# Performance work log

Measured on AMD Instinct MI355X. Metric: run time of the kernel, lower is better.

The kernel has to match this reference:

```python
import jax, jax.numpy as jnp
import numpy as np

IN_DIM = 4096
OUT_DIM = 4096
BLOCK = 256
RANK = 16
B_IN = IN_DIM // BLOCK   # 16
B_OUT = OUT_DIM // BLOCK # 16


def setup_inputs() -> dict:
    key = jax.random.key(0)
    k1, k2, k3, k4, k5 = jax.random.split(key, 5)
    x = jax.random.normal(k1, (2, 1024, IN_DIM), dtype=jnp.float32)
    # S ~ U[0, 2)
    S = jax.random.uniform(k2, (B_OUT, B_IN, RANK), dtype=jnp.float32, minval=0.0, maxval=2.0)
    std = np.sqrt(0.02).astype(np.float32)
    U = jax.random.normal(k3, (B_OUT, RANK, BLOCK), dtype=jnp.float32) * std
    Vt = jax.random.normal(k4, (B_IN, BLOCK, RANK), dtype=jnp.float32) * std
    # kaiming_uniform_ on a (1, out_dim) tensor with default a=sqrt(5): bound = 1/sqrt(fan_in) = 1/sqrt(out_dim)
    bound = float(1.0 / np.sqrt(OUT_DIM))
    bias = jax.random.uniform(k5, (OUT_DIM,), dtype=jnp.float32, minval=-bound, maxval=bound)
    return {"x": x, "S": S, "U": U, "Vt": Vt, "bias": bias}


def reference(x, S, U, Vt, bias):
    # Faithful to Blast.forward: it reconstructs the dense weight by running
    # forward2 on an identity matrix (which ALSO adds bias to every row of W),
    # then computes addmm(bias, x, W).
    # Block (i_in, i_out) of W0 = Vt[i_in] @ diag(S[i_out, i_in]) @ U[i_out].
    W0 = jnp.einsum('ipr,oir,orq->ipoq', Vt, S, U).reshape(IN_DIM, OUT_DIM)
    W = W0 + bias[None, :]  # identity-trick: forward2(I) adds bias to each of the in_dim rows
    out = x @ W + bias      # [B, S, out_dim]
    return out
```

## Files before the change

### kernel.cpp

```cpp
#include <hip/hip_runtime.h>

#define IN_DIM  4096
#define OUT_DIM 4096
#define RANK    16
#define NBLK    16
#define KDIM    256

typedef __attribute__((ext_vector_type(8))) __bf16 bf16x8;
typedef __attribute__((ext_vector_type(4))) float  f32x4;
typedef __attribute__((ext_vector_type(4))) unsigned short u16x4;
typedef __attribute__((ext_vector_type(8))) unsigned short u16x8;

__device__ __forceinline__ unsigned short bf16_rne(float v) {
    unsigned u = __float_as_uint(v);
    unsigned r = (u + 0x7FFFu + ((u >> 16) & 1u)) >> 16;
    return (unsigned short)r;
}
__device__ __forceinline__ float bf16_f32(unsigned short h) {
    return __uint_as_float(((unsigned)h) << 16);
}


__global__ __launch_bounds__(256) void build_packB(const float* __restrict__ S,
                                                   const float* __restrict__ U,
                                                   u16x8* __restrict__ Bhi,
                                                   u16x8* __restrict__ Blo) {
    int t  = blockIdx.x * 256 + threadIdx.x;
    int c  = t & 15;
    int ko = (t >> 4) & 31;
    int nt = t >> 9;
    int o  = nt >> 4;
    int i  = ko >> 1;
    int q  = ((nt & 15) << 4) | c;
    int r0 = (ko & 1) << 3;
    const float* Sp = S + ((o * NBLK + i) * RANK + r0);
    const float* Up = U + (size_t)o * RANK * 256 + q;
    u16x8 hi, lo;
#pragma unroll
    for (int j = 0; j < 8; ++j) {
        float w = Sp[j] * Up[(size_t)(r0 + j) * 256];
        unsigned short h = bf16_rne(w);
        hi[j] = h;
        lo[j] = bf16_rne(w - bf16_f32(h));
    }
    Bhi[t] = hi;
    Blo[t] = lo;
}

__global__ __launch_bounds__(256) void factor_x(const float* __restrict__ x,
                                                const float* __restrict__ Vt,
                                                u16x4* __restrict__ Ahi4,
                                                u16x4* __restrict__ Alo4,
                                                float* __restrict__ rowsum_p,
                                                int M) {
    __shared__ float xs[64][129];
    __shared__ float ps[4][64][17];
    const int tid  = threadIdx.x;
    const int lane = tid & 63;
    const int w    = __builtin_amdgcn_readfirstlane(tid >> 6);
    const int i    = blockIdx.y;
    const int m0   = blockIdx.x * 64;
    const float* __restrict__ vt = Vt + (size_t)i * 256 * RANK;

    float acc[16];
#pragma unroll
    for (int r = 0; r < RANK; ++r) acc[r] = 0.0f;
    float rs = 0.0f;

#pragma unroll
    for (int ch = 0; ch < 2; ++ch) {
#pragma unroll
        for (int e = 0; e < 8; ++e) {
            int f   = e * 256 + tid;
            int row = f >> 5;
            int c4  = f & 31;
            float4 v = *reinterpret_cast<const float4*>(
                x + (size_t)(m0 + row) * IN_DIM + i * 256 + ch * 128 + c4 * 4);
            xs[row][c4 * 4 + 0] = v.x;
            xs[row][c4 * 4 + 1] = v.y;
            xs[row][c4 * 4 + 2] = v.z;
            xs[row][c4 * 4 + 3] = v.w;
        }
        __syncthreads();
        const int p0 = w * 32;
#pragma unroll 8
        for (int p = 0; p < 32; ++p) {
            float xv = xs[lane][p0 + p];
            rs += xv;
            const float* vp = vt + (size_t)(ch * 128 + p0 + p) * RANK;
#pragma unroll
            for (int r = 0; r < RANK; ++r) acc[r] = fmaf(xv, vp[r], acc[r]);
        }
        __syncthreads();
    }

#pragma unroll
    for (int r = 0; r < RANK; ++r) ps[w][lane][r] = acc[r];
    ps[w][lane][16] = rs;
    __syncthreads();

    const int m  = lane;
    const int rg = w;
    float v4[4];
#pragma unroll
    for (int rr = 0; rr < 4; ++rr) {
        int r = rg * 4 + rr;
        v4[rr] = ps[0][m][r] + ps[1][m][r] + ps[2][m][r] + ps[3][m][r];
    }
    const int gm = m0 + m;
    const int mt = gm >> 4, cc = gm & 15;
    const int ko = 2 * i + (rg >> 1);
    const int j0 = (rg & 1) * 4;
    u16x4 hi, lo;
#pragma unroll
    for (int rr = 0; rr < 4; ++rr) {
        unsigned short h = bf16_rne(v4[rr]);
        hi[rr] = h;
        lo[rr] = bf16_rne(v4[rr] - bf16_f32(h));
    }
    size_t off8 = (size_t)(mt * 32 + ko) * 16 + cc;
    Ahi4[off8 * 2 + (j0 >> 2)] = hi;
    Alo4[off8 * 2 + (j0 >> 2)] = lo;
    if (rg == 0) {
        float t = ps[0][m][16] + ps[1][m][16] + ps[2][m][16] + ps[3][m][16];
        rowsum_p[(size_t)i * M + gm] = t;
    }
}

__global__ __launch_bounds__(256) void rowsum_reduce(const float* __restrict__ rowsum_p,
                                                     float* __restrict__ rstot, int M) {
    int m = blockIdx.x * 256 + threadIdx.x;
    float s = 1.0f;
#pragma unroll
    for (int i = 0; i < NBLK; ++i) s += rowsum_p[(size_t)i * M + m];
    rstot[m] = s;
}

__global__ __launch_bounds__(256) void apply_mfma(const bf16x8* __restrict__ Ahi,
                                                  const bf16x8* __restrict__ Alo,
                                                  const bf16x8* __restrict__ Bhi,
                                                  const bf16x8* __restrict__ Blo,
                                                  const float* __restrict__ rstot,
                                                  const float* __restrict__ bias,
                                                  float* __restrict__ out, int M) {
    const int mblocks = M >> 6;
    const int nb  = blockIdx.x;
    const int q   = gridDim.x >> 3;
    const int lg  = (nb & 7) * q + (nb >> 3);
    const int mr  = lg % mblocks;
    const int nc  = lg / mblocks;
    const int m0  = mr * 64, n0 = nc * 256;

    const int tid = threadIdx.x;
    const int l   = tid & 63;
    const int wid = __builtin_amdgcn_readfirstlane(tid >> 6);
    const int wm  = wid & 1, wn = wid >> 1;
    const int kq  = l >> 4, c = l & 15;

    f32x4 acc[2][8];
#pragma unroll
    for (int f = 0; f < 2; ++f)
#pragma unroll
        for (int nf = 0; nf < 8; ++nf) acc[f][nf] = f32x4{0.f, 0.f, 0.f, 0.f};

    const int mtb = (m0 >> 4) + wm * 2;
    const int ntb = nc * 16 + wn * 8;

#pragma unroll 2
    for (int s = 0; s < 8; ++s) {
        const int kb = 4 * s + kq;
        bf16x8 ah[2], al[2];
#pragma unroll
        for (int f = 0; f < 2; ++f) {
            size_t off = (size_t)((mtb + f) * 32 + kb) * 16 + c;
            ah[f] = Ahi[off];
            al[f] = Alo[off];
        }
#pragma unroll
        for (int nf = 0; nf < 8; ++nf) {
            size_t off = (size_t)((ntb + nf) * 32 + kb) * 16 + c;
            bf16x8 bh = Bhi[off];
            bf16x8 bl = Blo[off];
#pragma unroll
            for (int f = 0; f < 2; ++f) {
                acc[f][nf] = __builtin_amdgcn_mfma_f32_16x16x32_bf16(ah[f], bh, acc[f][nf], 0, 0, 0);
                acc[f][nf] = __builtin_amdgcn_mfma_f32_16x16x32_bf16(ah[f], bl, acc[f][nf], 0, 0, 0);
                acc[f][nf] = __builtin_amdgcn_mfma_f32_16x16x32_bf16(al[f], bh, acc[f][nf], 0, 0, 0);
            }
        }
    }

#pragma unroll
    for (int f = 0; f < 2; ++f) {
        const int rowb = m0 + wm * 32 + f * 16 + kq * 4;
        float rsv[4];
#pragma unroll
        for (int reg = 0; reg < 4; ++reg) rsv[reg] = rstot[rowb + reg];
#pragma unroll
        for (int nf = 0; nf < 8; ++nf) {
            const int n = n0 + wn * 128 + nf * 16 + c;
            const float bv = bias[n];
#pragma unroll
            for (int reg = 0; reg < 4; ++reg)
                out[(size_t)(rowb + reg) * OUT_DIM + n] = acc[f][nf][reg] + rsv[reg] * bv;
        }
    }
}

extern "C" void kernel_launch(void* const* d_in, const int* in_sizes, int n_in,
                              void* d_out, int out_size, void* d_ws, size_t ws_size,
                              hipStream_t stream) {
    const float* x    = (const float*)d_in[0];
    const float* S    = (const float*)d_in[1];
    const float* U    = (const float*)d_in[2];
    const float* Vt   = (const float*)d_in[3];
    const float* bias = (const float*)d_in[4];
    float* out = (float*)d_out;
    const int M = in_sizes[0] / IN_DIM;

    char* ws = (char*)d_ws;
    u16x8* Bhi      = (u16x8*)ws;
    u16x8* Blo      = (u16x8*)(ws + (2u << 20));
    u16x8* Ahi      = (u16x8*)(ws + (4u << 20));
    u16x8* Alo      = (u16x8*)(ws + (5u << 20));
    float* rowsum_p = (float*)(ws + (6u << 20));
    float* rstot    = (float*)(ws + (6u << 20) + NBLK * M * 4);

    build_packB<<<512, 256, 0, stream>>>(S, U, Bhi, Blo);
    factor_x<<<dim3(M / 64, NBLK), 256, 0, stream>>>(x, Vt, (u16x4*)Ahi, (u16x4*)Alo,
                                                     rowsum_p, M);
    rowsum_reduce<<<M / 256, 256, 0, stream>>>(rowsum_p, rstot, M);
    apply_mfma<<<(M / 64) * (OUT_DIM / 256), 256, 0, stream>>>(
        reinterpret_cast<const bf16x8*>(Ahi), reinterpret_cast<const bf16x8*>(Alo),
        reinterpret_cast<const bf16x8*>(Bhi), reinterpret_cast<const bf16x8*>(Blo),
        rstot, bias, out, M);
}
```

Baseline: 115.9 us.

## Compute x·Vt factor with split-bf16 MFMA and fold rowsum reduction into apply

Replaces the scalar-FMA factor_x kernel, which staged x through LDS, with a per-wave MFMA kernel. Each wave computes a 16-row by 16-rank tile using split-bf16 (hi/lo) operands, with Vt pre-split into bf16 packs inside a merged pack-building kernel. The separate rowsum_reduce launch is removed: apply_mfma now sums the partial row sums into shared memory at block start. This cuts one launch and the scalar FMA cost, but each apply block repeats the 16-way rowsum read and three-term split-bf16 may shift accuracy slightly.

```diff
diff --git a/kernel.cpp b/kernel.cpp
--- a/kernel.cpp
+++ b/kernel.cpp
@@ -7,140 +7,127 @@
 #define KDIM    256
 
 typedef __attribute__((ext_vector_type(8))) __bf16 bf16x8;
+typedef __attribute__((ext_vector_type(4))) __bf16 bf16x4;
 typedef __attribute__((ext_vector_type(4))) float  f32x4;
-typedef __attribute__((ext_vector_type(4))) unsigned short u16x4;
-typedef __attribute__((ext_vector_type(8))) unsigned short u16x8;
-
-__device__ __forceinline__ unsigned short bf16_rne(float v) {
-    unsigned u = __float_as_uint(v);
-    unsigned r = (u + 0x7FFFu + ((u >> 16) & 1u)) >> 16;
-    return (unsigned short)r;
-}
-__device__ __forceinline__ float bf16_f32(unsigned short h) {
-    return __uint_as_float(((unsigned)h) << 16);
-}
-
-
-__global__ __launch_bounds__(256) void build_packB(const float* __restrict__ S,
+
+
+__device__ __forceinline__ void split_bf16(float v, __bf16& h, __bf16& l) {
+    h = (__bf16)v;
+    l = (__bf16)(v - (float)h);
+}
+
+__global__ __launch_bounds__(256) void build_packs(const float* __restrict__ S,
                                                    const float* __restrict__ U,
-                                                   u16x8* __restrict__ Bhi,
-                                                   u16x8* __restrict__ Blo) {
-    int t  = blockIdx.x * 256 + threadIdx.x;
-    int c  = t & 15;
-    int ko = (t >> 4) & 31;
-    int nt = t >> 9;
-    int o  = nt >> 4;
-    int i  = ko >> 1;
-    int q  = ((nt & 15) << 4) | c;
-    int r0 = (ko & 1) << 3;
-    const float* Sp = S + ((o * NBLK + i) * RANK + r0);
-    const float* Up = U + (size_t)o * RANK * 256 + q;
-    u16x8 hi, lo;
-#pragma unroll
-    for (int j = 0; j < 8; ++j) {
-        float w = Sp[j] * Up[(size_t)(r0 + j) * 256];
-        unsigned short h = bf16_rne(w);
-        hi[j] = h;
-        lo[j] = bf16_rne(w - bf16_f32(h));
-    }
-    Bhi[t] = hi;
-    Blo[t] = lo;
-}
-
-__global__ __launch_bounds__(256) void factor_x(const float* __restrict__ x,
-                                                const float* __restrict__ Vt,
-                                                u16x4* __restrict__ Ahi4,
-                                                u16x4* __restrict__ Alo4,
-                                                float* __restrict__ rowsum_p,
-                                                int M) {
-    __shared__ float xs[64][129];
-    __shared__ float ps[4][64][17];
-    const int tid  = threadIdx.x;
-    const int lane = tid & 63;
-    const int w    = __builtin_amdgcn_readfirstlane(tid >> 6);
-    const int i    = blockIdx.y;
-    const int m0   = blockIdx.x * 64;
-    const float* __restrict__ vt = Vt + (size_t)i * 256 * RANK;
-
-    float acc[16];
-#pragma unroll
-    for (int r = 0; r < RANK; ++r) acc[r] = 0.0f;
-    float rs = 0.0f;
-
-#pragma unroll
-    for (int ch = 0; ch < 2; ++ch) {
-#pragma unroll
-        for (int e = 0; e < 8; ++e) {
-            int f   = e * 256 + tid;
-            int row = f >> 5;
-            int c4  = f & 31;
-            float4 v = *reinterpret_cast<const float4*>(
-                x + (size_t)(m0 + row) * IN_DIM + i * 256 + ch * 128 + c4 * 4);
-            xs[row][c4 * 4 + 0] = v.x;
-            xs[row][c4 * 4 + 1] = v.y;
-            xs[row][c4 * 4 + 2] = v.z;
-            xs[row][c4 * 4 + 3] = v.w;
-        }
-        __syncthreads();
-        const int p0 = w * 32;
-#pragma unroll 8
-        for (int p = 0; p < 32; ++p) {
-            float xv = xs[lane][p0 + p];
-            rs += xv;
-            const float* vp = vt + (size_t)(ch * 128 + p0 + p) * RANK;
-#pragma unroll
-            for (int r = 0; r < RANK; ++r) acc[r] = fmaf(xv, vp[r], acc[r]);
-        }
-        __syncthreads();
-    }
-
-#pragma unroll
-    for (int r = 0; r < RANK; ++r) ps[w][lane][r] = acc[r];
-    ps[w][lane][16] = rs;
-    __syncthreads();
-
-    const int m  = lane;
-    const int rg = w;
-    float v4[4];
-#pragma unroll
-    for (int rr = 0; rr < 4; ++rr) {
-        int r = rg * 4 + rr;
-        v4[rr] = ps[0][m][r] + ps[1][m][r] + ps[2][m][r] + ps[3][m][r];
-    }
-    const int gm = m0 + m;
-    const int mt = gm >> 4, cc = gm & 15;
-    const int ko = 2 * i + (rg >> 1);
-    const int j0 = (rg & 1) * 4;
-    u16x4 hi, lo;
-#pragma unroll
-    for (int rr = 0; rr < 4; ++rr) {
-        unsigned short h = bf16_rne(v4[rr]);
-        hi[rr] = h;
-        lo[rr] = bf16_rne(v4[rr] - bf16_f32(h));
-    }
-    size_t off8 = (size_t)(mt * 32 + ko) * 16 + cc;
-    Ahi4[off8 * 2 + (j0 >> 2)] = hi;
-    Alo4[off8 * 2 + (j0 >> 2)] = lo;
-    if (rg == 0) {
-        float t = ps[0][m][16] + ps[1][m][16] + ps[2][m][16] + ps[3][m][16];
-        rowsum_p[(size_t)i * M + gm] = t;
-    }
-}
-
-__global__ __launch_bounds__(256) void rowsum_reduce(const float* __restrict__ rowsum_p,
-                                                     float* __restrict__ rstot, int M) {
-    int m = blockIdx.x * 256 + threadIdx.x;
-    float s = 1.0f;
-#pragma unroll
-    for (int i = 0; i < NBLK; ++i) s += rowsum_p[(size_t)i * M + m];
-    rstot[m] = s;
+                                                   const float* __restrict__ Vt,
+                                                   bf16x8* __restrict__ Bhi,
+                                                   bf16x8* __restrict__ Blo,
+                                                   bf16x8* __restrict__ Vhi,
+                                                   bf16x8* __restrict__ Vlo) {
+    const int blk = blockIdx.x;
+    if (blk < 512) {
+        int t  = blk * 256 + threadIdx.x;
+        int c  = t & 15;
+        int ko = (t >> 4) & 31;
+        int nt = t >> 9;
+        int o  = nt >> 4;
+        int i  = ko >> 1;
+        int q  = ((nt & 15) << 4) | c;
+        int r0 = (ko & 1) << 3;
+        const float* Sp = S + ((o * NBLK + i) * RANK + r0);
+        const float* Up = U + (size_t)o * RANK * 256 + q;
+        bf16x8 hi, lo;
+#pragma unroll
+        for (int j = 0; j < 8; ++j) {
+            float w = Sp[j] * Up[(size_t)(r0 + j) * 256];
+            __bf16 h, l;
+            split_bf16(w, h, l);
+            hi[j] = h; lo[j] = l;
+        }
+        Bhi[t] = hi;
+        Blo[t] = lo;
+    } else {
+        int t  = (blk - 512) * 256 + threadIdx.x;
+        int c  = t & 15;
+        int p0 = (t >> 4) << 3;
+        int i  = t >> 9;
+        int pbase = (p0 & 255);
+        const float* vp = Vt + ((size_t)(i * 256 + pbase)) * RANK + c;
+        bf16x8 hi, lo;
+#pragma unroll
+        for (int j = 0; j < 8; ++j) {
+            float w = vp[(size_t)j * RANK];
+            __bf16 h, l;
+            split_bf16(w, h, l);
+            hi[j] = h; lo[j] = l;
+        }
+        Vhi[t] = hi;
+        Vlo[t] = lo;
+    }
+}
+
+__global__ __launch_bounds__(256) void factor_mfma(const float* __restrict__ x,
+                                                   const bf16x8* __restrict__ Vhi,
+                                                   const bf16x8* __restrict__ Vlo,
+                                                   bf16x4* __restrict__ Ahi4,
+                                                   bf16x4* __restrict__ Alo4,
+                                                   float* __restrict__ rowsum_p,
+                                                   int M) {
+    const int tid = threadIdx.x;
+    const int l   = tid & 63;
+    const int w   = tid >> 6;
+    const int job = blockIdx.x * 4 + w;
+    const int i   = job & 15;
+    const int mt  = job >> 4;
+    const int row = l & 15;
+    const int qt  = l >> 4;
+
+    const float* xp = x + (size_t)(mt * 16 + row) * IN_DIM + i * 256 + qt * 8;
+
+    f32x4 acc = {0.f, 0.f, 0.f, 0.f};
+    float rs = 0.f;
+#pragma unroll
+    for (int ks = 0; ks < 8; ++ks) {
+        float4 a = *reinterpret_cast<const float4*>(xp + ks * 32);
+        float4 b = *reinterpret_cast<const float4*>(xp + ks * 32 + 4);
+        rs += (a.x + a.y) + (a.z + a.w) + (b.x + b.y) + (b.z + b.w);
+        float vv[8] = {a.x, a.y, a.z, a.w, b.x, b.y, b.z, b.w};
+        bf16x8 xh, xl;
+#pragma unroll
+        for (int jj = 0; jj < 8; ++jj) {
+            __bf16 h, lo_;
+            split_bf16(vv[jj], h, lo_);
+            xh[jj] = h; xl[jj] = lo_;
+        }
+        size_t vidx = (size_t)((i * 8 + ks) * 4 + qt) * 16 + row;
+        bf16x8 vh = Vhi[vidx];
+        bf16x8 vl = Vlo[vidx];
+        acc = __builtin_amdgcn_mfma_f32_16x16x32_bf16(vh, xh, acc, 0, 0, 0);
+        acc = __builtin_amdgcn_mfma_f32_16x16x32_bf16(vh, xl, acc, 0, 0, 0);
+        acc = __builtin_amdgcn_mfma_f32_16x16x32_bf16(vl, xh, acc, 0, 0, 0);
+    }
+
+    rs += __shfl_xor(rs, 16, 64);
+    rs += __shfl_xor(rs, 32, 64);
+    if (l < 16)
+        rowsum_p[(size_t)i * M + mt * 16 + l] = rs;
+
+    bf16x4 hi, lo;
+#pragma unroll
+    for (int reg = 0; reg < 4; ++reg) {
+        __bf16 h, lo_;
+        split_bf16(acc[reg], h, lo_);
+        hi[reg] = h; lo[reg] = lo_;
+    }
+    size_t o4 = ((size_t)(mt * 32 + i * 2 + (l >> 5)) * 16 + row) * 2 + ((l >> 4) & 1);
+    Ahi4[o4] = hi;
+    Alo4[o4] = lo;
 }
 
 __global__ __launch_bounds__(256) void apply_mfma(const bf16x8* __restrict__ Ahi,
                                                   const bf16x8* __restrict__ Alo,
                                                   const bf16x8* __restrict__ Bhi,
                                                   const bf16x8* __restrict__ Blo,
-                                                  const float* __restrict__ rstot,
+                                                  const float* __restrict__ rowsum_p,
                                                   const float* __restrict__ bias,
                                                   float* __restrict__ out, int M) {
     const int mblocks = M >> 6;
@@ -157,6 +144,15 @@
     const int wm  = wid & 1, wn = wid >> 1;
     const int kq  = l >> 4, c = l & 15;
 
+    __shared__ float rstot_s[64];
+    if (tid < 64) {
+        float s = 1.0f;
+#pragma unroll
+        for (int i = 0; i < NBLK; ++i) s += rowsum_p[(size_t)i * M + m0 + tid];
+        rstot_s[tid] = s;
+    }
+    __syncthreads();
+
     f32x4 acc[2][8];
 #pragma unroll
     for (int f = 0; f < 2; ++f)
@@ -192,10 +188,11 @@
 
 #pragma unroll
     for (int f = 0; f < 2; ++f) {
-        const int rowb = m0 + wm * 32 + f * 16 + kq * 4;
+        const int rloc = wm * 32 + f * 16 + kq * 4;
+        const int rowb = m0 + rloc;
         float rsv[4];
 #pragma unroll
-        for (int reg = 0; reg < 4; ++reg) rsv[reg] = rstot[rowb + reg];
+        for (int reg = 0; reg < 4; ++reg) rsv[reg] = rstot_s[rloc + reg];
 #pragma unroll
         for (int nf = 0; nf < 8; ++nf) {
             const int n = n0 + wn * 128 + nf * 16 + c;
@@ -219,19 +216,17 @@
     const int M = in_sizes[0] / IN_DIM;
 
     char* ws = (char*)d_ws;
-    u16x8* Bhi      = (u16x8*)ws;
-    u16x8* Blo      = (u16x8*)(ws + (2u << 20));
-    u16x8* Ahi      = (u16x8*)(ws + (4u << 20));
-    u16x8* Alo      = (u16x8*)(ws + (5u << 20));
-    float* rowsum_p = (float*)(ws + (6u << 20));
-    float* rstot    = (float*)(ws + (6u << 20) + NBLK * M * 4);
-
-    build_packB<<<512, 256, 0, stream>>>(S, U, Bhi, Blo);
-    factor_x<<<dim3(M / 64, NBLK), 256, 0, stream>>>(x, Vt, (u16x4*)Ahi, (u16x4*)Alo,
-                                                     rowsum_p, M);
-    rowsum_reduce<<<M / 256, 256, 0, stream>>>(rowsum_p, rstot, M);
+    bf16x8* Bhi     = (bf16x8*)ws;
+    bf16x8* Blo     = (bf16x8*)(ws + (2u << 20));
+    bf16x8* Ahi     = (bf16x8*)(ws + (4u << 20));
+    bf16x8* Alo     = (bf16x8*)(ws + (5u << 20));
+    bf16x8* Vhi     = (bf16x8*)(ws + (6u << 20));
+    bf16x8* Vlo     = (bf16x8*)(ws + (6u << 20) + (128u << 10));
+    float* rowsum_p = (float*)(ws + (6u << 20) + (256u << 10));
+
+    build_packs<<<544, 256, 0, stream>>>(S, U, Vt, Bhi, Blo, Vhi, Vlo);
+    factor_mfma<<<M / 4, 256, 0, stream>>>(x, Vhi, Vlo,
+                                           (bf16x4*)Ahi, (bf16x4*)Alo, rowsum_p, M);
     apply_mfma<<<(M / 64) * (OUT_DIM / 256), 256, 0, stream>>>(
-        reinterpret_cast<const bf16x8*>(Ahi), reinterpret_cast<const bf16x8*>(Alo),
-        reinterpret_cast<const bf16x8*>(Bhi), reinterpret_cast<const bf16x8*>(Blo),
-        rstot, bias, out, M);
-}
+        Ahi, Alo, Bhi, Blo, rowsum_p, bias, out, M);
+}
```

Measured after the change: 114.0 us. About the same (-1.7%).
